# Performance work log

Hardware: AMD Instinct MI355X
Metric: run time of the kernel (lower is better)

## Reference

```python
import jax, jax.numpy as jnp
import numpy as np

N_HEADS = 8
FACTOR = 5


def setup_inputs() -> dict:
    key = jax.random.key(0)
    ks = jax.random.split(key, 8)
    B, L, D = 2, 4096, 512
    sample_k = min(FACTOR * int(np.ceil(np.log(L))), L)  # 45
    inp = {
        "queries": jax.random.normal(ks[0], (B, L, D), jnp.float32),
        "keys": jax.random.normal(ks[1], (B, L, D), jnp.float32),
        "values": jax.random.normal(ks[2], (B, L, D), jnp.float32),
        "Wq": jax.random.normal(ks[3], (D, D), jnp.float32) * 0.02,
        "bq": jnp.zeros((D,), jnp.float32),
        "Wk": jax.random.normal(ks[4], (D, D), jnp.float32) * 0.02,
        "bk": jnp.zeros((D,), jnp.float32),
        "Wv": jax.random.normal(ks[5], (D, D), jnp.float32) * 0.02,
        "bv": jnp.zeros((D,), jnp.float32),
        "index_sample": jax.random.randint(ks[6], (L, sample_k), 0, L, jnp.int32),
    }
    return inp


def reference(queries, keys, values, Wq, bq, Wk, bk, Wv, bv, index_sample):
    b, l_q, d_model = queries.shape
    _, l_k, _ = keys.shape
    h = N_HEADS
    d = d_model // h
    # projections -> [b, h, l, d]
    q = (queries @ Wq + bq).reshape(b, l_q, h, d).transpose(0, 2, 1, 3)
    k = (keys @ Wk + bk).reshape(b, l_k, h, d).transpose(0, 2, 1, 3)
    v = (values @ Wv + bv).reshape(b, l_k, h, d).transpose(0, 2, 1, 3)
    n_top = min(FACTOR * int(np.ceil(np.log(l_q))), l_q)
    # --- prob_qk: sparse sampled QK ---
    # gather sampled keys per query position: [b, h, l_q, sample_k, d]
    k_sample = k[:, :, index_sample, :]
    q_k_sample = jnp.einsum('bhld,bhlsd->bhls', q, k_sample)
    # sparsity measure M(q, K) = max - mean
    m = q_k_sample.max(-1) - q_k_sample.sum(-1) / l_k  # [b, h, l_q]
    _, m_top = jax.lax.top_k(m, n_top)  # [b, h, n_top]
    q_reduce = jnp.take_along_axis(q, m_top[..., None], axis=2)  # [b, h, u, d]
    scores = jnp.einsum('bhud,bhkd->bhuk', q_reduce, k)  # [b, h, u, l_k]
    scale = float(1.0 / np.sqrt(d))
    scores = scores * scale
    # --- causal ProbMask on the selected query rows ---
    causal = jnp.triu(jnp.ones((l_q, l_k), bool), 1)
    mask = causal[m_top]  # [b, h, u, l_k]
    scores = jnp.where(mask, -jnp.inf, scores)
    attn = jax.nn.softmax(scores, axis=-1)
    # --- initial context: causal cumsum of V; scatter updated rows ---
    context = jnp.cumsum(v, axis=2)  # [b, h, l_q, d]
    upd = jnp.einsum('bhuk,bhkd->bhud', attn, v)
    bi = jnp.arange(b)[:, None, None]
    hi = jnp.arange(h)[None, :, None]
    context = context.at[bi, hi, m_top].set(upd)
    return context.transpose(0, 2, 1, 3).reshape(b, l_q, h * d)
```

## Files before the change

### kernel.cpp

```cpp
#include <hip/hip_runtime.h>
#include <math.h>

#define B  2
#define L  4096
#define D  512
#define H  8
#define DH 64
#define BH (B * H)
#define K3 1536
#define XPW 1024

typedef short s16x8 __attribute__((ext_vector_type(8)));
typedef float f32x4 __attribute__((ext_vector_type(4)));

#define AS1 __attribute__((address_space(1)))
#define AS3 __attribute__((address_space(3)))

__device__ __forceinline__ void lds_load16(const void* g, void* l) {
    __builtin_amdgcn_global_load_lds((const AS1 unsigned int*)g,
                                     (AS3 unsigned int*)l, 16, 0, 0);
}

__device__ __forceinline__ unsigned short f2bf(float x) {
    union { float f; unsigned u; } v; v.f = x;
    unsigned u = v.u;
    return (unsigned short)((u + 0x7fff + ((u >> 16) & 1)) >> 16);
}
__device__ __forceinline__ float bf2f(unsigned short h) {
    union { float f; unsigned u; } v; v.u = ((unsigned)h) << 16;
    return v.f;
}

#define MEMFENCE asm volatile("" ::: "memory")
__device__ __forceinline__ void wg_bar() {
    MEMFENCE;
    __builtin_amdgcn_s_barrier();
    MEMFENCE;
}

__global__ __launch_bounds__(256)
void k_split(const float* __restrict__ q, const float* __restrict__ k,
             const float* __restrict__ v,
             const float* __restrict__ wq, const float* __restrict__ wk,
             const float* __restrict__ wv,
             unsigned short* __restrict__ Xp, unsigned short* __restrict__ WpT)
{
    const int tid = threadIdx.x;
    if (blockIdx.x < 192) {
        __shared__ float t[64][65];
        const int bx = blockIdx.x;
        const int e  = bx >> 6;
        const int k0 = (bx & 7) * 64;
        const int n0 = ((bx >> 3) & 7) * 64;
        const float* W = (e == 0) ? wq : (e == 1) ? wk : wv;

        for (int idx = tid; idx < 64 * 16; idx += 256) {
            const int i = idx >> 4, j4 = (idx & 15) << 2;
            *(float4*)&t[i][j4] = *(const float4*)(W + (size_t)(k0 + i) * 512 + n0 + j4);
        }
        __syncthreads();

        const int n_loc = tid >> 2;
        const int kq    = (tid & 3) << 4;
        unsigned short h[16], l[16];
        #pragma unroll
        for (int tt = 0; tt < 16; tt++) {
            const float x = t[kq + tt][n_loc];
            h[tt] = f2bf(x);
            l[tt] = f2bf(x - bf2f(h[tt]));
        }
        unsigned short* base = WpT + (size_t)e * 512 * K3 + (size_t)(n0 + n_loc) * K3 + k0 + kq;
        #pragma unroll
        for (int g4 = 0; g4 < 4; g4++) {
            ushort4 hv = make_ushort4(h[g4*4], h[g4*4+1], h[g4*4+2], h[g4*4+3]);
            ushort4 lv = make_ushort4(l[g4*4], l[g4*4+1], l[g4*4+2], l[g4*4+3]);
            *(ushort4*)(base + g4*4)        = hv;
            *(ushort4*)(base + 512 + g4*4)  = lv;
            *(ushort4*)(base + 1024 + g4*4) = hv;
        }
    } else {
        const size_t g = (size_t)(blockIdx.x - 192) * 256 + tid;
        const size_t per = (size_t)8192 * 128;
        const int e = (int)(g / per);
        const size_t rem = g - (size_t)e * per;
        const int m  = (int)(rem >> 7);
        const int kq = (int)(rem & 127) << 2;

        const float* X = (e == 0) ? q : (e == 1) ? k : v;
        const float4 x = *(const float4*)(X + (size_t)m * 512 + kq);

        unsigned short h0 = f2bf(x.x), h1 = f2bf(x.y), h2 = f2bf(x.z), h3 = f2bf(x.w);
        unsigned short* dst = Xp + (size_t)e * 8192 * XPW + (size_t)m * XPW + kq;
        *(ushort4*)(dst) = make_ushort4(h0, h1, h2, h3);
        if (e != 2) {
            unsigned short l0 = f2bf(x.x - bf2f(h0)), l1 = f2bf(x.y - bf2f(h1));
            unsigned short l2 = f2bf(x.z - bf2f(h2)), l3 = f2bf(x.w - bf2f(h3));
            *(ushort4*)(dst + 512) = make_ushort4(l0, l1, l2, l3);
        }
    }
}

#define MFMA16 __builtin_amdgcn_mfma_f32_16x16x32_bf16

__global__ __launch_bounds__(512, 2)
void gemm_mfma(const unsigned short* __restrict__ Xp,
               const unsigned short* __restrict__ WpT,
               const float* __restrict__ bq, const float* __restrict__ bk,
               const float* __restrict__ bv,
               float* __restrict__ Qo, float* __restrict__ Ko,
               float* __restrict__ Vo)
{
    __shared__ __align__(16) unsigned short lds[65536];

    const int e = blockIdx.z;
    const float* bias = (e == 0) ? bq : (e == 1) ? bk : bv;
    float* C          = (e == 0) ? Qo : (e == 1) ? Ko : Vo;
    const unsigned short* Ag = Xp  + (size_t)e * 8192 * XPW;
    const unsigned short* Bg = WpT + (size_t)e * 512 * K3;
    const int NT = (e == 2) ? 8 : 24;

    const int tid  = threadIdx.x;
    const int lane = tid & 63;
    const int wid  = tid >> 6;
    const int wm   = wid & 1;
    const int wn   = wid >> 1;
    const int m0   = blockIdx.x * 256;
    const int n0g  = blockIdx.y * 256;

    const int srow = wid * 8 + (lane >> 3);
    const int scq8 = ((lane & 7) ^ (lane >> 3)) << 3;
    const unsigned short* aSrc = Ag + (size_t)(m0 + srow) * XPW + scq8;
    const unsigned short* bSrc = Bg + (size_t)(n0g + srow) * K3 + scq8;
    unsigned short* ldsA = lds;
    unsigned short* ldsB = lds + 32768;
    unsigned short* dA = ldsA + wid * 512;
    unsigned short* dB = ldsB + wid * 512;

    const int r16 = lane & 15, quad = lane >> 4;
    const int x3 = r16 & 7;
    const int c0 = ((quad ^ x3) << 4);
    const int c1 = (((4 | quad) ^ x3) << 4);
    const char* fA = (const char*)ldsA + (wm * 128 + r16) * 128;
    const char* fB = (const char*)ldsB + (wn * 64 + r16) * 128;

    f32x4 acc[8][4];
    #pragma unroll
    for (int i = 0; i < 8; i++)
        #pragma unroll
        for (int j = 0; j < 4; j++)
            acc[i][j] = (f32x4){0.f, 0.f, 0.f, 0.f};

    #pragma unroll
    for (int j = 0; j < 4; j++)
        lds_load16(aSrc + (size_t)(j * 64) * XPW, dA + j * 4096);
    #pragma unroll
    for (int j = 0; j < 4; j++)
        lds_load16(bSrc + (size_t)(j * 64) * K3, dB + j * 4096);

    s16x8 aF[8], b0[4], b1[4];

    for (int t = 0; t < NT; ++t) {
        const int pa = (t & 1) << 15;
        const int na = (~t & 1) * 16384;

        if (t + 1 < NT) {
            const int k1 = (t + 1) * 64;
            const int ka = (k1 < 512) ? k1 : k1 - 512;
            #pragma unroll
            for (int j = 0; j < 4; j++)
                lds_load16(aSrc + (size_t)(j * 64) * XPW + ka, dA + na + j * 4096);
            #pragma unroll
            for (int j = 0; j < 4; j++)
                lds_load16(bSrc + (size_t)(j * 64) * K3 + k1, dB + na + j * 4096);
            asm volatile("s_waitcnt vmcnt(8)" ::: "memory");
        } else {
            asm volatile("s_waitcnt vmcnt(0)" ::: "memory");
        }
        wg_bar();

        #pragma unroll
        for (int mq = 0; mq < 4; mq++) {
            aF[mq * 2]     = *(const s16x8*)(fA + pa + mq * 2048 + c0);
            aF[mq * 2 + 1] = *(const s16x8*)(fA + pa + mq * 2048 + c1);
        }
        #pragma unroll
        for (int nq = 0; nq < 2; nq++) {
            b0[nq * 2]     = *(const s16x8*)(fB + pa + nq * 2048 + c0);
            b0[nq * 2 + 1] = *(const s16x8*)(fB + pa + nq * 2048 + c1);
            b1[nq * 2]     = *(const s16x8*)(fB + pa + (2 + nq) * 2048 + c0);
            b1[nq * 2 + 1] = *(const s16x8*)(fB + pa + (2 + nq) * 2048 + c1);
        }
        __builtin_amdgcn_s_setprio(1);
        #pragma unroll
        for (int mq = 0; mq < 4; mq++)
            #pragma unroll
            for (int nq = 0; nq < 2; nq++) {
                acc[mq][nq]   = MFMA16(aF[mq*2],   b0[nq*2],   acc[mq][nq],   0, 0, 0);
                acc[mq][nq]   = MFMA16(aF[mq*2+1], b0[nq*2+1], acc[mq][nq],   0, 0, 0);
                acc[mq][2+nq] = MFMA16(aF[mq*2],   b1[nq*2],   acc[mq][2+nq], 0, 0, 0);
                acc[mq][2+nq] = MFMA16(aF[mq*2+1], b1[nq*2+1], acc[mq][2+nq], 0, 0, 0);
            }
        __builtin_amdgcn_s_setprio(0);

        #pragma unroll
        for (int mq = 0; mq < 4; mq++) {
            aF[mq * 2]     = *(const s16x8*)(fA + pa + 8192 + mq * 2048 + c0);
            aF[mq * 2 + 1] = *(const s16x8*)(fA + pa + 8192 + mq * 2048 + c1);
        }
        __builtin_amdgcn_s_setprio(1);
        #pragma unroll
        for (int mq = 0; mq < 4; mq++)
            #pragma unroll
            for (int nq = 0; nq < 2; nq++) {
                acc[4+mq][nq]   = MFMA16(aF[mq*2],   b0[nq*2],   acc[4+mq][nq],   0, 0, 0);
                acc[4+mq][nq]   = MFMA16(aF[mq*2+1], b0[nq*2+1], acc[4+mq][nq],   0, 0, 0);
                acc[4+mq][2+nq] = MFMA16(aF[mq*2],   b1[nq*2],   acc[4+mq][2+nq], 0, 0, 0);
                acc[4+mq][2+nq] = MFMA16(aF[mq*2+1], b1[nq*2+1], acc[4+mq][2+nq], 0, 0, 0);
            }
        __builtin_amdgcn_s_setprio(0);
        wg_bar();
    }

    #pragma unroll
    for (int nt = 0; nt < 4; nt++) {
        const int col = n0g + wn * 64 + nt * 16 + r16;
        const float bb = bias[col];
        #pragma unroll
        for (int mt = 0; mt < 8; mt++) {
            const int row0 = m0 + wm * 128 + mt * 16 + quad * 4;
            #pragma unroll
            for (int i = 0; i < 4; i++)
                C[(size_t)(row0 + i) * 512 + col] = acc[mt][nt][i] + bb;
        }
    }
}

#define CH 64
__global__ __launch_bounds__(256)
void k_sample_chunks(const float* __restrict__ Q, const float* __restrict__ K,
                     const int* __restrict__ idx, float* __restrict__ m_out, int S,
                     const float* __restrict__ V, float* __restrict__ partial)
{
    const int tid = threadIdx.x;
    if (blockIdx.x < 256) {
        const int bid = blockIdx.x;
        const int c  = (bid & 15) * 4 + (tid >> 6);
        const int h  = (bid >> 4) & (H - 1);
        const int b  = bid >> 7;
        const int d  = tid & 63;
        const float* base = V + (size_t)b * L * D + h * DH + d + (size_t)(c * CH) * D;

        float vals[CH];
        #pragma unroll
        for (int i = 0; i < CH; i++) vals[i] = base[(size_t)i * D];

        float s0 = 0.f, s1 = 0.f, s2 = 0.f, s3 = 0.f;
        #pragma unroll
        for (int i = 0; i < CH; i += 4) {
            s0 += vals[i]; s1 += vals[i+1]; s2 += vals[i+2]; s3 += vals[i+3];
        }
        partial[((size_t)((b * H + h) * 64 + c)) * DH + d] = (s0 + s1) + (s2 + s3);
    } else {
        const int lane = tid & 63;
        const int wib  = tid >> 6;
        const int i    = blockIdx.x - 256;
        const int bh   = i & 15;
        const int lg   = i >> 4;
        const int l = lg * 4 + wib;
        const int h = bh & (H - 1);
        const int b = bh >> 3;
        const int widx = (bh << 12) | l;

        const int r4 = lane >> 2;
        const int c4 = lane & 3;

        float4 qf[4];
        {
            const float4* qv = (const float4*)(Q + ((size_t)b * L + l) * D + h * DH);
            #pragma unroll
            for (int ii = 0; ii < 4; ii++) qf[ii] = qv[c4 + 4 * ii];
        }

        const float* Kb = K + (size_t)b * L * D + h * DH;
        const int* is = idx + (size_t)l * S;

        int  jj[3];
        bool ok[3];
        #pragma unroll
        for (int p = 0; p < 3; p++) {
            const int sp = p * 16 + r4;
            ok[p] = sp < S;
            jj[p] = ok[p] ? is[sp] : 0;
        }
        float4 kv[3][4];
        #pragma unroll
        for (int p = 0; p < 3; p++) {
            const float4* Krow = (const float4*)(Kb + (size_t)jj[p] * D);
            #pragma unroll
            for (int ii = 0; ii < 4; ii++) kv[p][ii] = Krow[c4 + 4 * ii];
        }

        float vmax = -INFINITY, vsum = 0.f;
        #pragma unroll
        for (int p = 0; p < 3; p++) {
            float dot = 0.f;
            #pragma unroll
            for (int ii = 0; ii < 4; ii++) {
                const float4 kvv = kv[p][ii];
                const float4 qq = qf[ii];
                dot += qq.x * kvv.x + qq.y * kvv.y + qq.z * kvv.z + qq.w * kvv.w;
            }
            dot += __shfl_xor(dot, 1, 64);
            dot += __shfl_xor(dot, 2, 64);
            if (ok[p]) {
                vmax = fmaxf(vmax, dot);
                if (c4 == 0) vsum += dot;
            }
        }
        #pragma unroll
        for (int off = 32; off >= 4; off >>= 1) {
            vmax = fmaxf(vmax, __shfl_xor(vmax, off, 64));
            vsum += __shfl_xor(vsum, off, 64);
        }
        if (lane == 0) m_out[widx] = vmax - vsum * (1.0f / (float)L);
    }
}

__global__ __launch_bounds__(256)
void topk_kernel(const float* __restrict__ m_in, int* __restrict__ m_top,
                 float* __restrict__ sums, int* __restrict__ flags, int NT)
{
    __shared__ unsigned hist[256];
    __shared__ unsigned sfx[257];
    __shared__ int sh_b, sh_rem;
    __shared__ int cnt_gt, cnt_eq;
    __shared__ int eqlist[128];

    const float* m = m_in + (size_t)blockIdx.x * L;
    const int tid = threadIdx.x;
    int* out = m_top + blockIdx.x * NT;
    int* fl  = flags + (size_t)blockIdx.x * L;

    if (tid < NT) sums[blockIdx.x * NT + tid] = 0.f;
    for (int i = tid; i < L; i += 256) fl[i] = 0;

    unsigned uv[16];
    #pragma unroll
    for (int k = 0; k < 16; k++) {
        const float f = m[tid + k * 256];
        const unsigned x = __float_as_uint(f);
        uv[k] = (x & 0x80000000u) ? ~x : (x | 0x80000000u);
    }

    unsigned prefix = 0;
    int rem = NT;

    for (int level = 0; level < 4; level++) {
        const int shift = 24 - level * 8;
        hist[tid] = 0;
        if (tid == 0) { cnt_gt = 0; cnt_eq = 0; }
        __syncthreads();
        #pragma unroll
        for (int k = 0; k < 16; k++) {
            const bool part = (level == 0) || ((uv[k] >> (shift + 8)) == prefix);
            if (part) atomicAdd(&hist[(uv[k] >> shift) & 255], 1u);
        }
        __syncthreads();
        if (tid < 64) {
            const unsigned s0 = hist[4*tid+0], s1 = hist[4*tid+1];
            const unsigned s2 = hist[4*tid+2], s3 = hist[4*tid+3];
            const unsigned loc = s0 + s1 + s2 + s3;
            unsigned suf = loc;
            #pragma unroll
            for (int off = 1; off < 64; off <<= 1) {
                const unsigned t = __shfl_down(suf, off, 64);
                if (tid + off < 64) suf += t;
            }
            const unsigned tail = suf - loc;
            sfx[4*tid+3] = tail + s3;
            sfx[4*tid+2] = tail + s3 + s2;
            sfx[4*tid+1] = tail + s3 + s2 + s1;
            sfx[4*tid+0] = suf;
            if (tid == 0) sfx[256] = 0;
        }
        __syncthreads();
        if (sfx[tid + 1] < (unsigned)rem && (unsigned)rem <= sfx[tid]) {
            sh_b   = tid;
            sh_rem = rem - (int)sfx[tid + 1];
        }
        __syncthreads();
        prefix = (prefix << 8) | (unsigned)sh_b;
        rem    = sh_rem;
        __syncthreads();
    }

    const unsigned T = prefix;
    const int n_gt = NT - rem;

    #pragma unroll
    for (int k = 0; k < 16; k++) {
        if (uv[k] > T) {
            const int pos = atomicAdd(&cnt_gt, 1);
            out[pos] = tid + k * 256;
        } else if (uv[k] == T) {
            const int pos = atomicAdd(&cnt_eq, 1);
            if (pos < 128) eqlist[pos] = tid + k * 256;
        }
    }
    __syncthreads();
    if (tid == 0) {
        int n = cnt_eq < 128 ? cnt_eq : 128;
        for (int r = 0; r < rem; r++) {
            int best = 0x7fffffff, bi = 0;
            for (int i = 0; i < n; i++)
                if (eqlist[i] < best) { best = eqlist[i]; bi = i; }
            out[n_gt + r] = best;
            eqlist[bi] = 0x7fffffff;
        }
    }
    __syncthreads();
    if (tid < NT) fl[out[tid]] = 1;
}

__global__ __launch_bounds__(256)
void k_cumsum_scores(const float* __restrict__ V, const float* __restrict__ partial,
                     const int* __restrict__ flags, float* __restrict__ out,
                     const float* __restrict__ Q, const float* __restrict__ K,
                     const int* __restrict__ m_top, float* __restrict__ scores,
                     float* __restrict__ sums, int NT)
{
    const int tid = threadIdx.x;
    if (blockIdx.x < 256) {
        const int bid = blockIdx.x;
        const int c  = (bid & 15) * 4 + (tid >> 6);
        const int h  = (bid >> 4) & (H - 1);
        const int b  = bid >> 7;
        const int d  = tid & 63;
        const size_t off = (size_t)b * L * D + h * DH + d + (size_t)(c * CH) * D;
        const float* base  = V   + off;
        float*       obase = out + off;
        const float* pb = partial + (size_t)((b * H + h) * 64) * DH + d;
        const int*   fp = flags + (size_t)(b * H + h) * L + c * CH;

        float vals[CH];
        #pragma unroll
        for (int i = 0; i < CH; i++) vals[i] = base[(size_t)i * D];

        float acc = 0.f;
        for (int cc = 0; cc < c; cc++) acc += pb[cc * DH];

        #pragma unroll
        for (int i = 0; i < CH; i++) {
            acc += vals[i];
            obase[(size_t)i * D] = fp[i] ? 0.f : acc;
        }
    } else {
        __shared__ float qsh[15][DH];
        __shared__ int   psh[15];

        const int rem2 = blockIdx.x - 256;
        const int bh = rem2 / 24;
        const int r2 = rem2 % 24;
        const int ug = r2 >> 3;
        const int jc = r2 & 7;
        const int h  = bh & (H - 1);
        const int b  = bh >> 3;
        const int j0 = jc * 512;

        for (int i = tid; i < 15 * DH; i += 256) {
            const int u = i >> 6, d = i & 63;
            const int p = m_top[bh * NT + ug * 15 + u];
            if (d == 0) psh[u] = p;
            qsh[u][d] = Q[((size_t)b * L + p) * D + h * DH + d];
        }
        __syncthreads();

        const float* Kb = K + (size_t)b * L * D + h * DH;
        const int ja = j0 + tid;
        const int jb = ja + 256;
        float4 k0[16], k1[16];
        {
            const float4* ra = (const float4*)(Kb + (size_t)ja * D);
            const float4* rb = (const float4*)(Kb + (size_t)jb * D);
            #pragma unroll
            for (int i = 0; i < 16; i++) { k0[i] = ra[i]; k1[i] = rb[i]; }
        }

        for (int u = 0; u < 15; u++) {
            const int p = psh[u];
            const float4* qv = (const float4*)qsh[u];
            float d0 = 0.f, d1 = 0.f;
            #pragma unroll
            for (int i = 0; i < 16; i++) {
                const float4 q4 = qv[i];
                d0 += q4.x * k0[i].x + q4.y * k0[i].y + q4.z * k0[i].z + q4.w * k0[i].w;
                d1 += q4.x * k1[i].x + q4.y * k1[i].y + q4.z * k1[i].z + q4.w * k1[i].w;
            }
            const float e0 = (ja <= p) ? __expf(d0 * 0.125f) : 0.f;
            const float e1 = (jb <= p) ? __expf(d1 * 0.125f) : 0.f;
            float* srow = scores + (size_t)(bh * NT + ug * 15 + u) * L;
            srow[ja] = e0;
            srow[jb] = e1;
            float t = e0 + e1;
            #pragma unroll
            for (int off = 32; off; off >>= 1) t += __shfl_xor(t, off, 64);
            if ((tid & 63) == 0) atomicAdd(&sums[bh * NT + ug * 15 + u], t);
        }
    }
}

__global__ __launch_bounds__(256)
void attn_wv(const float* __restrict__ scores, const float* __restrict__ V,
             const int* __restrict__ m_top, const float* __restrict__ sums,
             float* __restrict__ out, int NT)
{
    __shared__ float ssh[45][64];
    __shared__ float sinv[45];
    __shared__ int   psh[45];

    const int bh = blockIdx.y;
    const int h  = bh & (H - 1);
    const int b  = bh >> 3;
    const int j0 = blockIdx.x * 64;
    const int tid = threadIdx.x;
    const int d   = tid & 63;
    const int w   = tid >> 6;

    if (tid < NT) {
        psh[tid]  = m_top[bh * NT + tid];
        sinv[tid] = 1.0f / sums[bh * NT + tid];
    }

    const float* Vb = V + (size_t)b * L * D + h * DH + d;
    float vreg[64];
    #pragma unroll
    for (int i = 0; i < 64; i++) vreg[i] = Vb[(size_t)(j0 + i) * D];

    __syncthreads();
    for (int i = tid; i < NT * 64; i += 256) {
        const int u = i >> 6, j = i & 63;
        ssh[u][j] = scores[(size_t)(bh * NT + u) * L + j0 + j] * sinv[u];
    }
    __syncthreads();

    for (int u = w; u < NT; u += 4) {
        const int p = psh[u];
        if (p < j0) continue;
        const float* wt = ssh[u];
        float acc = 0.f;
        #pragma unroll
        for (int i = 0; i < 64; i++) acc += wt[i] * vreg[i];
        atomicAdd(out + ((size_t)b * L + p) * D + h * DH + d, acc);
    }
}

extern "C" void kernel_launch(void* const* d_in, const int* in_sizes, int n_in,
                              void* d_out, int out_size, void* d_ws, size_t ws_size,
                              hipStream_t stream)
{
    const float* queries = (const float*)d_in[0];
    const float* keys    = (const float*)d_in[1];
    const float* values  = (const float*)d_in[2];
    const float* Wq      = (const float*)d_in[3];
    const float* bq      = (const float*)d_in[4];
    const float* Wk      = (const float*)d_in[5];
    const float* bk      = (const float*)d_in[6];
    const float* Wv      = (const float*)d_in[7];
    const float* bv      = (const float*)d_in[8];
    const int*   idx     = (const int*)d_in[9];
    float* out = (float*)d_out;

    const int S  = in_sizes[9] / L;
    const int NT = S;

    const size_t NE = (size_t)B * L * D;
    float* Qb      = (float*)d_ws;
    float* Kb      = Qb + NE;
    float* Vb      = Kb + NE;
    float* m_buf   = Vb + NE;
    float* cs_part = m_buf + (size_t)BH * L;
    int*   m_top   = (int*)(cs_part + (size_t)BH * 64 * DH);
    float* sums    = (float*)(m_top + 1024);
    int*   flags   = (int*)(sums + 1024);
    float* scores  = (float*)(flags + (size_t)BH * L);
    unsigned short* Xp  = (unsigned short*)(scores + (size_t)BH * NT * L);
    unsigned short* WpT = Xp + (size_t)3 * 8192 * XPW;

    k_split<<<192 + 3 * 8192 * 128 / 256, 256, 0, stream>>>(
        queries, keys, values, Wq, Wk, Wv, Xp, WpT);

    gemm_mfma<<<dim3(8192 / 256, 512 / 256, 3), 512, 0, stream>>>(
        Xp, WpT, bq, bk, bv, Qb, Kb, Vb);

    k_sample_chunks<<<256 + BH * L / 4, 256, 0, stream>>>(
        Qb, Kb, idx, m_buf, S, Vb, cs_part);

    topk_kernel<<<BH, 256, 0, stream>>>(m_buf, m_top, sums, flags, NT);

    k_cumsum_scores<<<256 + 384, 256, 0, stream>>>(
        Vb, cs_part, flags, out, Qb, Kb, m_top, scores, sums, NT);

    attn_wv<<<dim3(64, BH), 256, 0, stream>>>(scores, Vb, m_top, sums, out, NT);
}
```

Before: 266.7 us.

## Restructure split-bf16 projection GEMM to reuse A-hi fragments across hi/lo products

The Q/K projection GEMM previously treated the three-term split-bf16 product (Ah·Bh, Al·Bh, Ah·Bl) as one K=1536 reduction, streaming duplicated hi data through the concatenated K dimension. Now each K step of 32 stages Ah, Al, Bh and Bl tiles together and runs three MFMA passes from registers, so A-hi and B-hi are loaded once and reused. This removes the redundant third weight copy in prep and reorganises the LDS layout and swizzle for 32-wide K tiles. The cost is more LDS loads per barrier and a new swizzle pattern that could introduce bank conflicts.

Measured after the change: 262.2 us. Within noise of the previous version (-1.7%).

```diff
diff --git a/kernel.cpp b/kernel.cpp
--- a/kernel.cpp
+++ b/kernel.cpp
@@ -76,7 +76,6 @@
             ushort4 lv = make_ushort4(l[g4*4], l[g4*4+1], l[g4*4+2], l[g4*4+3]);
             *(ushort4*)(base + g4*4)        = hv;
             *(ushort4*)(base + 512 + g4*4)  = lv;
-            *(ushort4*)(base + 1024 + g4*4) = hv;
         }
     } else {
         const size_t g = (size_t)(blockIdx.x - 192) * 256 + tid;
@@ -117,7 +116,6 @@
     float* C          = (e == 0) ? Qo : (e == 1) ? Ko : Vo;
     const unsigned short* Ag = Xp  + (size_t)e * 8192 * XPW;
     const unsigned short* Bg = WpT + (size_t)e * 512 * K3;
-    const int NT = (e == 2) ? 8 : 24;
 
     const int tid  = threadIdx.x;
     const int lane = tid & 63;
@@ -127,21 +125,27 @@
     const int m0   = blockIdx.x * 256;
     const int n0g  = blockIdx.y * 256;
 
-    const int srow = wid * 8 + (lane >> 3);
-    const int scq8 = ((lane & 7) ^ (lane >> 3)) << 3;
-    const unsigned short* aSrc = Ag + (size_t)(m0 + srow) * XPW + scq8;
-    const unsigned short* bSrc = Bg + (size_t)(n0g + srow) * K3 + scq8;
-    unsigned short* ldsA = lds;
-    unsigned short* ldsB = lds + 32768;
-    unsigned short* dA = ldsA + wid * 512;
-    unsigned short* dB = ldsB + wid * 512;
+    const int srow = lane >> 2;
+    const int spos = lane & 3;
+    const int sswz = (spos ^ ((srow >> 1) & 3)) << 3;
+    const int row0 = wid * 32 + srow;
+    const int row1 = row0 + 16;
+
+    const unsigned short* aH0 = Ag + (size_t)(m0 + row0) * XPW + sswz;
+    const unsigned short* aH1 = Ag + (size_t)(m0 + row1) * XPW + sswz;
+    const unsigned short* aL0 = aH0 + 512;
+    const unsigned short* aL1 = aH1 + 512;
+    const unsigned short* bH0 = Bg + (size_t)(n0g + row0) * K3 + sswz;
+    const unsigned short* bH1 = Bg + (size_t)(n0g + row1) * K3 + sswz;
+    const unsigned short* bL0 = bH0 + 512;
+    const unsigned short* bL1 = bH1 + 512;
+
+    const int wr0 = wid * 1024;
+    const int wr1 = wr0 + 512;
 
     const int r16 = lane & 15, quad = lane >> 4;
-    const int x3 = r16 & 7;
-    const int c0 = ((quad ^ x3) << 4);
-    const int c1 = (((4 | quad) ^ x3) << 4);
-    const char* fA = (const char*)ldsA + (wm * 128 + r16) * 128;
-    const char* fB = (const char*)ldsB + (wn * 64 + r16) * 128;
+    const int laneOff = r16 * 64 + ((quad ^ ((r16 >> 1) & 3)) << 4);
+    const char* ldsC = (const char*)lds;
 
     f32x4 acc[8][4];
     #pragma unroll
@@ -150,75 +154,113 @@
         for (int j = 0; j < 4; j++)
             acc[i][j] = (f32x4){0.f, 0.f, 0.f, 0.f};
 
-    #pragma unroll
-    for (int j = 0; j < 4; j++)
-        lds_load16(aSrc + (size_t)(j * 64) * XPW, dA + j * 4096);
-    #pragma unroll
-    for (int j = 0; j < 4; j++)
-        lds_load16(bSrc + (size_t)(j * 64) * K3, dB + j * 4096);
-
-    s16x8 aF[8], b0[4], b1[4];
-
-    for (int t = 0; t < NT; ++t) {
-        const int pa = (t & 1) << 15;
-        const int na = (~t & 1) * 16384;
-
-        if (t + 1 < NT) {
-            const int k1 = (t + 1) * 64;
-            const int ka = (k1 < 512) ? k1 : k1 - 512;
-            #pragma unroll
-            for (int j = 0; j < 4; j++)
-                lds_load16(aSrc + (size_t)(j * 64) * XPW + ka, dA + na + j * 4096);
-            #pragma unroll
-            for (int j = 0; j < 4; j++)
-                lds_load16(bSrc + (size_t)(j * 64) * K3 + k1, dB + na + j * 4096);
-            asm volatile("s_waitcnt vmcnt(8)" ::: "memory");
-        } else {
-            asm volatile("s_waitcnt vmcnt(0)" ::: "memory");
-        }
-        wg_bar();
-
-        #pragma unroll
-        for (int mq = 0; mq < 4; mq++) {
-            aF[mq * 2]     = *(const s16x8*)(fA + pa + mq * 2048 + c0);
-            aF[mq * 2 + 1] = *(const s16x8*)(fA + pa + mq * 2048 + c1);
-        }
-        #pragma unroll
-        for (int nq = 0; nq < 2; nq++) {
-            b0[nq * 2]     = *(const s16x8*)(fB + pa + nq * 2048 + c0);
-            b0[nq * 2 + 1] = *(const s16x8*)(fB + pa + nq * 2048 + c1);
-            b1[nq * 2]     = *(const s16x8*)(fB + pa + (2 + nq) * 2048 + c0);
-            b1[nq * 2 + 1] = *(const s16x8*)(fB + pa + (2 + nq) * 2048 + c1);
-        }
-        __builtin_amdgcn_s_setprio(1);
-        #pragma unroll
-        for (int mq = 0; mq < 4; mq++)
-            #pragma unroll
-            for (int nq = 0; nq < 2; nq++) {
-                acc[mq][nq]   = MFMA16(aF[mq*2],   b0[nq*2],   acc[mq][nq],   0, 0, 0);
-                acc[mq][nq]   = MFMA16(aF[mq*2+1], b0[nq*2+1], acc[mq][nq],   0, 0, 0);
-                acc[mq][2+nq] = MFMA16(aF[mq*2],   b1[nq*2],   acc[mq][2+nq], 0, 0, 0);
-                acc[mq][2+nq] = MFMA16(aF[mq*2+1], b1[nq*2+1], acc[mq][2+nq], 0, 0, 0);
+    const int NT = 16;
+
+    if (e != 2) {
+        #define STAGE_QK(kk, nu) do {                                   \
+            const int ka_ = (kk) * 32;                                  \
+            unsigned short* dd_ = lds + (nu);                           \
+            lds_load16(aH0 + ka_, dd_ + wr0);                           \
+            lds_load16(aH1 + ka_, dd_ + wr1);                           \
+            lds_load16(aL0 + ka_, dd_ + 8192  + wr0);                   \
+            lds_load16(aL1 + ka_, dd_ + 8192  + wr1);                   \
+            lds_load16(bH0 + ka_, dd_ + 16384 + wr0);                   \
+            lds_load16(bH1 + ka_, dd_ + 16384 + wr1);                   \
+            lds_load16(bL0 + ka_, dd_ + 24576 + wr0);                   \
+            lds_load16(bL1 + ka_, dd_ + 24576 + wr1);                   \
+        } while (0)
+
+        STAGE_QK(0, 0);
+        s16x8 aF[8], bh[4], bl[4];
+
+        for (int t = 0; t < NT; ++t) {
+            const int pa = (t & 1) << 16;
+            const int nu = (~t & 1) << 15;
+            if (t + 1 < NT) {
+                STAGE_QK(t + 1, nu);
+                asm volatile("s_waitcnt vmcnt(8)" ::: "memory");
+            } else {
+                asm volatile("s_waitcnt vmcnt(0)" ::: "memory");
             }
-        __builtin_amdgcn_s_setprio(0);
-
-        #pragma unroll
-        for (int mq = 0; mq < 4; mq++) {
-            aF[mq * 2]     = *(const s16x8*)(fA + pa + 8192 + mq * 2048 + c0);
-            aF[mq * 2 + 1] = *(const s16x8*)(fA + pa + 8192 + mq * 2048 + c1);
-        }
-        __builtin_amdgcn_s_setprio(1);
-        #pragma unroll
-        for (int mq = 0; mq < 4; mq++)
-            #pragma unroll
-            for (int nq = 0; nq < 2; nq++) {
-                acc[4+mq][nq]   = MFMA16(aF[mq*2],   b0[nq*2],   acc[4+mq][nq],   0, 0, 0);
-                acc[4+mq][nq]   = MFMA16(aF[mq*2+1], b0[nq*2+1], acc[4+mq][nq],   0, 0, 0);
-                acc[4+mq][2+nq] = MFMA16(aF[mq*2],   b1[nq*2],   acc[4+mq][2+nq], 0, 0, 0);
-                acc[4+mq][2+nq] = MFMA16(aF[mq*2+1], b1[nq*2+1], acc[4+mq][2+nq], 0, 0, 0);
+            wg_bar();
+
+            const char* base = ldsC + pa;
+            const char* fAh = base + (wm * 128) * 64 + laneOff;
+            const char* fAl = base + 16384 + (wm * 128) * 64 + laneOff;
+            const char* fBh = base + 32768 + (wn * 64) * 64 + laneOff;
+            const char* fBl = base + 49152 + (wn * 64) * 64 + laneOff;
+
+            #pragma unroll
+            for (int mq = 0; mq < 8; mq++) aF[mq] = *(const s16x8*)(fAh + mq * 1024);
+            #pragma unroll
+            for (int nq = 0; nq < 4; nq++) {
+                bh[nq] = *(const s16x8*)(fBh + nq * 1024);
+                bl[nq] = *(const s16x8*)(fBl + nq * 1024);
             }
-        __builtin_amdgcn_s_setprio(0);
-        wg_bar();
+            __builtin_amdgcn_s_setprio(1);
+            #pragma unroll
+            for (int mq = 0; mq < 8; mq++)
+                #pragma unroll
+                for (int nq = 0; nq < 4; nq++)
+                    acc[mq][nq] = MFMA16(aF[mq], bh[nq], acc[mq][nq], 0, 0, 0);
+            #pragma unroll
+            for (int mq = 0; mq < 8; mq++)
+                #pragma unroll
+                for (int nq = 0; nq < 4; nq++)
+                    acc[mq][nq] = MFMA16(aF[mq], bl[nq], acc[mq][nq], 0, 0, 0);
+            __builtin_amdgcn_s_setprio(0);
+
+            #pragma unroll
+            for (int mq = 0; mq < 8; mq++) aF[mq] = *(const s16x8*)(fAl + mq * 1024);
+            __builtin_amdgcn_s_setprio(1);
+            #pragma unroll
+            for (int mq = 0; mq < 8; mq++)
+                #pragma unroll
+                for (int nq = 0; nq < 4; nq++)
+                    acc[mq][nq] = MFMA16(aF[mq], bh[nq], acc[mq][nq], 0, 0, 0);
+            __builtin_amdgcn_s_setprio(0);
+            wg_bar();
+        }
+    } else {
+        #define STAGE_V(kk, nu) do {                                    \
+            const int ka_ = (kk) * 32;                                  \
+            unsigned short* dd_ = lds + (nu);                           \
+            lds_load16(aH0 + ka_, dd_ + wr0);                           \
+            lds_load16(aH1 + ka_, dd_ + wr1);                           \
+            lds_load16(bH0 + ka_, dd_ + 16384 + wr0);                   \
+            lds_load16(bH1 + ka_, dd_ + 16384 + wr1);                   \
+        } while (0)
+
+        STAGE_V(0, 0);
+        s16x8 aF[8], bh[4];
+
+        for (int t = 0; t < NT; ++t) {
+            const int pa = (t & 1) << 16;
+            const int nu = (~t & 1) << 15;
+            if (t + 1 < NT) {
+                STAGE_V(t + 1, nu);
+                asm volatile("s_waitcnt vmcnt(4)" ::: "memory");
+            } else {
+                asm volatile("s_waitcnt vmcnt(0)" ::: "memory");
+            }
+            wg_bar();
+
+            const char* base = ldsC + pa;
+            const char* fAh = base + (wm * 128) * 64 + laneOff;
+            const char* fBh = base + 32768 + (wn * 64) * 64 + laneOff;
+            #pragma unroll
+            for (int mq = 0; mq < 8; mq++) aF[mq] = *(const s16x8*)(fAh + mq * 1024);
+            #pragma unroll
+            for (int nq = 0; nq < 4; nq++) bh[nq] = *(const s16x8*)(fBh + nq * 1024);
+            __builtin_amdgcn_s_setprio(1);
+            #pragma unroll
+            for (int mq = 0; mq < 8; mq++)
+                #pragma unroll
+                for (int nq = 0; nq < 4; nq++)
+                    acc[mq][nq] = MFMA16(aF[mq], bh[nq], acc[mq][nq], 0, 0, 0);
+            __builtin_amdgcn_s_setprio(0);
+            wg_bar();
+        }
     }
 
     #pragma unroll
@@ -227,10 +269,10 @@
         const float bb = bias[col];
         #pragma unroll
         for (int mt = 0; mt < 8; mt++) {
-            const int row0 = m0 + wm * 128 + mt * 16 + quad * 4;
+            const int row0e = m0 + wm * 128 + mt * 16 + quad * 4;
             #pragma unroll
             for (int i = 0; i < 4; i++)
-                C[(size_t)(row0 + i) * 512 + col] = acc[mt][nt][i] + bb;
+                C[(size_t)(row0e + i) * 512 + col] = acc[mt][nt][i] + bb;
         }
     }
 }
```
